# Kernel tuning notes

Hardware: AMD Instinct MI355X
Metric: run time of the kernel (lower is better)

The kernel has to match this reference:

```python
import jax, jax.numpy as jnp
import numpy as np

EPS = 1e-5

def _layernorm(x, g, b):
    # normalize over last (channel) axis
    mu = jnp.mean(x, axis=-1, keepdims=True)
    var = jnp.var(x, axis=-1, keepdims=True)
    return (x - mu) * jax.lax.rsqrt(var + EPS) * g + b

def _dynamix(xt, wnd, bnd, wnn, bnn):
    # xt: [B, M, N, C]; mixes over the N axis (vectorized form of the per-slice loop)
    B, M, N, C = xt.shape
    d = wnd.shape[1]
    p = xt @ wnd + bnd                       # [B,M,N,d]
    p = p.reshape(B, M, N * d) @ wnn + bnn   # [B,M,N*N]
    p = jax.nn.softmax(p.reshape(B, M, N, N), axis=-1)
    return jnp.einsum('bmij,bmjc->bmic', p, xt)  # [B,M,N,C]

def setup_inputs() -> dict:
    key = jax.random.key(0)
    ks = jax.random.split(key, 10)
    B, C, H, W, d, E = 32, 128, 56, 56, 10, 4
    def n(k, shape, scale=0.02):
        return jax.random.normal(k, shape, jnp.float32) * scale
    return {
        'x': jax.random.normal(ks[0], (B, C, H, W), jnp.float32),
        'ln1_g': jnp.ones((C,), jnp.float32), 'ln1_b': jnp.zeros((C,), jnp.float32),
        'h_wnd': n(ks[1], (C, d)), 'h_bnd': jnp.zeros((d,), jnp.float32),
        'h_wnn': n(ks[2], (W * d, W * W)), 'h_bnn': jnp.zeros((W * W,), jnp.float32),
        'w_wnd': n(ks[3], (C, d)), 'w_bnd': jnp.zeros((d,), jnp.float32),
        'w_wnn': n(ks[4], (H * d, H * H)), 'w_bnn': jnp.zeros((H * H,), jnp.float32),
        'pc_w': n(ks[5], (C, C)), 'pc_b': jnp.zeros((C,), jnp.float32),
        'po_w': n(ks[6], (C, C)), 'po_b': jnp.zeros((C,), jnp.float32),
        'ln2_g': jnp.ones((C,), jnp.float32), 'ln2_b': jnp.zeros((C,), jnp.float32),
        'fc1_w': n(ks[7], (C, E * C)), 'fc1_b': jnp.zeros((E * C,), jnp.float32),
        'fc2_w': n(ks[8], (E * C, C)), 'fc2_b': jnp.zeros((C,), jnp.float32),
    }

def reference(x, ln1_g, ln1_b, h_wnd, h_bnd, h_wnn, h_bnn,
              w_wnd, w_bnd, w_wnn, w_bnn, pc_w, pc_b, po_w, po_b,
              ln2_g, ln2_b, fc1_w, fc1_b, fc2_w, fc2_b):
    # x: [B,C,H,W] -> work channels-last [B,H,W,C]
    xt = jnp.transpose(x, (0, 2, 3, 1))
    # ---- block p1: LN + DynaMixer ----
    u = _layernorm(xt, ln1_g, ln1_b)                 # [B,H,W,C]
    y_h = _dynamix(u, h_wnd, h_bnd, h_wnn, h_bnn)    # mix over W per row
    u_w = jnp.transpose(u, (0, 2, 1, 3))             # [B,W,H,C]
    y_w = _dynamix(u_w, w_wnd, w_bnd, w_wnn, w_bnn)  # mix over H per col
    y_w = jnp.transpose(y_w, (0, 2, 1, 3))           # back to [B,H,W,C]
    y_c = u @ pc_w + pc_b                            # 1x1 conv proj_c
    y = (y_h + y_w + y_c) @ po_w + po_b              # 1x1 conv proj_o
    xt = xt + y                                      # residual (drop_path=0)
    # ---- block p2: LN + MLP ----
    v = _layernorm(xt, ln2_g, ln2_b)
    h = jax.nn.gelu(v @ fc1_w + fc1_b, approximate=False)
    h = h @ fc2_w + fc2_b
    xt = xt + h
    return jnp.transpose(xt, (0, 3, 1, 2))           # [B,C,H,W]
```

## Files before the change

### kernel.cpp

```cpp
#include <hip/hip_runtime.h>
#include <math.h>

#define BB 32
#define CC 128
#define HH 56
#define WW 56
#define HWHW 3136
#define TOK 100352
#define BH 1792
#define NDP 576
#define NNP 3200

typedef __attribute__((ext_vector_type(8))) short bhalf8;
typedef __attribute__((ext_vector_type(4))) float f32x4;
typedef __attribute__((ext_vector_type(4))) unsigned int u32x4;

__device__ inline unsigned short f2bf(float f) {
  unsigned int x = __float_as_uint(f);
  unsigned int r = (x + 0x7FFFu + ((x >> 16) & 1u)) >> 16;
  return (unsigned short)r;
}
__device__ inline float bf2f(unsigned short u) {
  return __uint_as_float(((unsigned int)u) << 16);
}
__device__ inline unsigned int pack2(float a, float b) {
  return (unsigned int)f2bf(a) | ((unsigned int)f2bf(b) << 16);
}
__device__ inline f32x4 MFMA(bhalf8 a, bhalf8 b, f32x4 c) {
  return __builtin_amdgcn_mfma_f32_16x16x32_bf16(a, b, c, 0, 0, 0);
}
template <int CH>
__device__ inline bhalf8 ldsFrag(const unsigned short* base, int row, int chunk) {
  return *reinterpret_cast<const bhalf8*>(base + row * (CH * 8) + ((chunk ^ (row & 7)) * 8));
}
__device__ inline float gelu_f(float x) {
  float x3 = x * x * x;
  float z = 0.7978845608028654f * (x + 0.044715f * x3);
  float e = __expf(2.0f * z);
  float t = 1.0f - 2.0f / (e + 1.0f);
  return 0.5f * x * (1.0f + t);
}

__global__ __launch_bounds__(256) void wcvt_kernel(
    const float* __restrict__ hwnn, const float* __restrict__ wwnn,
    const float* __restrict__ pcw, const float* __restrict__ pow_,
    const float* __restrict__ fc1w, const float* __restrict__ fc2w,
    const float* __restrict__ hwnd, const float* __restrict__ wwnd,
    unsigned short* __restrict__ wnnTh, unsigned short* __restrict__ wnnTw,
    unsigned short* __restrict__ pcT, unsigned short* __restrict__ poT,
    unsigned short* __restrict__ fc1T, unsigned short* __restrict__ fc2T,
    unsigned short* __restrict__ wcatT, u32x4* __restrict__ pdzero) {
  int gt = blockIdx.x * 256 + threadIdx.x;
  int gs = gridDim.x * 256;
  for (int i = gt; i < 258048; i += gs) { u32x4 z = {0, 0, 0, 0}; pdzero[i] = z; }
  for (int i = gt; i < 3200 * 576; i += gs) {
    int k = i / 3200, n = i % 3200;
    float v = (n < 3136 && k < 560) ? hwnn[(size_t)k * 3136 + n] : 0.f;
    wnnTh[(size_t)n * 576 + k] = f2bf(v);
  }
  for (int i = gt; i < 3200 * 576; i += gs) {
    int k = i / 3200, n = i % 3200;
    float v = (n < 3136 && k < 560) ? wwnn[(size_t)k * 3136 + n] : 0.f;
    wnnTw[(size_t)n * 576 + k] = f2bf(v);
  }
  for (int i = gt; i < 128 * 128; i += gs) { int k = i >> 7, n = i & 127; pcT[n * 128 + k] = f2bf(pcw[i]); }
  for (int i = gt; i < 128 * 128; i += gs) { int k = i >> 7, n = i & 127; poT[n * 128 + k] = f2bf(pow_[i]); }
  for (int i = gt; i < 128 * 512; i += gs) { int k = i >> 9, n = i & 511; fc1T[n * 128 + k] = f2bf(fc1w[i]); }
  for (int i = gt; i < 512 * 128; i += gs) { int k = i >> 7, n = i & 127; fc2T[n * 512 + k] = f2bf(fc2w[i]); }
  for (int i = gt; i < 128 * 32; i += gs) {
    int k = i >> 5, n = i & 31;
    float v = n < 10 ? hwnd[k * 10 + n] : (n < 20 ? wwnd[k * 10 + (n - 10)] : 0.f);
    wcatT[n * 128 + k] = f2bf(v);
  }
}

__global__ __launch_bounds__(256) void ln1_kernel(const float* __restrict__ x,
    const float* __restrict__ g, const float* __restrict__ bt,
    unsigned short* __restrict__ ubf, unsigned short* __restrict__ xcl) {
  int bh = blockIdx.x;
  int b = bh / HH, h = bh % HH;
  __shared__ float lds[WW][CC + 1];
  __shared__ float mu[WW], rs[WW];
  const float* xp = x + ((size_t)b * CC) * HWHW + (size_t)h * WW;
  for (int idx = threadIdx.x; idx < CC * WW; idx += 256) {
    int c = idx / WW, w = idx % WW;
    lds[w][c] = xp[(size_t)c * HWHW + w];
  }
  __syncthreads();
  if (threadIdx.x < WW) {
    int w = threadIdx.x;
    float s = 0.f, ss = 0.f;
    for (int c = 0; c < CC; ++c) { float v = lds[w][c]; s += v; ss += v * v; }
    float m = s * (1.0f / CC);
    float var = ss * (1.0f / CC) - m * m;
    mu[w] = m; rs[w] = rsqrtf(var + 1e-5f);
  }
  __syncthreads();
  unsigned short* up = ubf + (size_t)bh * (WW * CC);
  unsigned short* xc = xcl + (size_t)bh * (WW * CC);
  for (int idx = threadIdx.x; idx < WW * CC; idx += 256) {
    int w = idx >> 7, c = idx & 127;
    float v = lds[w][c];
    up[idx] = f2bf((v - mu[w]) * rs[w] * g[c] + bt[c]);
    xc[idx] = f2bf(v);
  }
}

__global__ __launch_bounds__(256) void pd_mfma(const unsigned short* __restrict__ ubf,
    const unsigned short* __restrict__ wcatT, const float* __restrict__ hbnd,
    const float* __restrict__ wbnd, unsigned short* __restrict__ pdh,
    unsigned short* __restrict__ pdw) {
  __shared__ __align__(16) unsigned short sU[64 * 128];
  __shared__ __align__(16) unsigned short sW[32 * 128];
  int tid = threadIdx.x;
  int tok0 = blockIdx.x * 64;
  #pragma unroll
  for (int i = 0; i < 4; ++i) {
    int s = i * 256 + tid; int r = s >> 4, c = s & 15;
    u32x4 v = *reinterpret_cast<const u32x4*>(ubf + (size_t)(tok0 + r) * 128 + c * 8);
    *reinterpret_cast<u32x4*>(sU + r * 128 + ((c ^ (r & 7)) * 8)) = v;
  }
  #pragma unroll
  for (int i = 0; i < 2; ++i) {
    int s = i * 256 + tid; int r = s >> 4, c = s & 15;
    u32x4 v = *reinterpret_cast<const u32x4*>(wcatT + (size_t)r * 128 + c * 8);
    *reinterpret_cast<u32x4*>(sW + r * 128 + ((c ^ (r & 7)) * 8)) = v;
  }
  __syncthreads();
  int wid = tid >> 6, lane = tid & 63, l16 = lane & 15, lk = lane >> 4;
  f32x4 acc[2] = {};
  #pragma unroll
  for (int kk = 0; kk < 4; ++kk) {
    bhalf8 a = ldsFrag<16>(sU, wid * 16 + l16, kk * 4 + lk);
    #pragma unroll
    for (int f = 0; f < 2; ++f) {
      bhalf8 b = ldsFrag<16>(sW, f * 16 + l16, kk * 4 + lk);
      acc[f] = MFMA(a, b, acc[f]);
    }
  }
  #pragma unroll
  for (int f = 0; f < 2; ++f) {
    int n = f * 16 + l16;
    #pragma unroll
    for (int r = 0; r < 4; ++r) {
      int tok = tok0 + wid * 16 + lk * 4 + r;
      float v = acc[f][r];
      if (n < 10) {
        pdh[((size_t)(tok / 56)) * NDP + (size_t)(tok % 56) * 10 + n] = f2bf(v + hbnd[n]);
      } else if (n < 20) {
        int b = tok / HWHW; int rem = tok % HWHW; int hh = rem / 56; int w = rem % 56;
        pdw[((size_t)(b * 56 + w)) * NDP + (size_t)hh * 10 + (n - 10)] = f2bf(v + wbnd[n - 10]);
      }
    }
  }
}

__global__ __launch_bounds__(256) void gemm_logits(
    const unsigned short* __restrict__ A, const unsigned short* __restrict__ BT,
    const float* __restrict__ bias, unsigned short* __restrict__ Cout) {
  __shared__ __align__(16) unsigned short sA[128 * 64];
  __shared__ __align__(16) unsigned short sB[128 * 64];
  int tid = threadIdx.x;
  int row0 = blockIdx.y * 128, col0 = blockIdx.x * 128;
  int wid = tid >> 6, lane = tid & 63;
  int wm = wid >> 1, wn = wid & 1;
  int l16 = lane & 15, lk = lane >> 4;
  f32x4 acc[4][4] = {};
  for (int k0 = 0; k0 < NDP; k0 += 64) {
    #pragma unroll
    for (int i = 0; i < 4; ++i) {
      int s = i * 256 + tid; int r = s >> 3, c = s & 7;
      u32x4 v = *reinterpret_cast<const u32x4*>(A + (size_t)(row0 + r) * NDP + k0 + c * 8);
      *reinterpret_cast<u32x4*>(sA + r * 64 + ((c ^ (r & 7)) * 8)) = v;
    }
    #pragma unroll
    for (int i = 0; i < 4; ++i) {
      int s = i * 256 + tid; int r = s >> 3, c = s & 7;
      u32x4 v = *reinterpret_cast<const u32x4*>(BT + (size_t)(col0 + r) * NDP + k0 + c * 8);
      *reinterpret_cast<u32x4*>(sB + r * 64 + ((c ^ (r & 7)) * 8)) = v;
    }
    __syncthreads();
    bhalf8 af[4][2], bf[4][2];
    #pragma unroll
    for (int f = 0; f < 4; ++f)
      #pragma unroll
      for (int kk = 0; kk < 2; ++kk) {
        af[f][kk] = ldsFrag<8>(sA, wm * 64 + f * 16 + l16, kk * 4 + lk);
        bf[f][kk] = ldsFrag<8>(sB, wn * 64 + f * 16 + l16, kk * 4 + lk);
      }
    #pragma unroll
    for (int i = 0; i < 4; ++i)
      #pragma unroll
      for (int j = 0; j < 4; ++j) {
        acc[i][j] = MFMA(af[i][0], bf[j][0], acc[i][j]);
        acc[i][j] = MFMA(af[i][1], bf[j][1], acc[i][j]);
      }
    __syncthreads();
  }
  #pragma unroll
  for (int i = 0; i < 4; ++i) {
    int rbase = row0 + wm * 64 + i * 16 + lk * 4;
    #pragma unroll
    for (int j = 0; j < 4; ++j) {
      int col = col0 + wn * 64 + j * 16 + l16;
      if (col < HWHW) {
        float bv = bias[col];
        #pragma unroll
        for (int r = 0; r < 4; ++r)
          Cout[(size_t)(rbase + r) * NNP + col] = f2bf(acc[i][j][r] + bv);
      }
    }
  }
}

__global__ __launch_bounds__(256) void softmax56_kernel(unsigned short* __restrict__ ph,
                                                        unsigned short* __restrict__ pw) {
  int wave = (blockIdx.x * 256 + threadIdx.x) >> 6;
  int lane = threadIdx.x & 63;
  if (wave >= 2 * TOK) return;
  unsigned short* buf = wave < TOK ? ph : pw;
  int row = wave < TOK ? wave : wave - TOK;
  int bh = row / 56, i = row % 56;
  unsigned short* p = buf + (size_t)bh * NNP + (size_t)i * 56;
  float xv = lane < WW ? bf2f(p[lane]) : -INFINITY;
  float m = xv;
  for (int o = 32; o > 0; o >>= 1) m = fmaxf(m, __shfl_xor(m, o));
  float e = lane < WW ? __expf(xv - m) : 0.f;
  float s = e;
  for (int o = 32; o > 0; o >>= 1) s += __shfl_xor(s, o);
  if (lane < WW) p[lane] = f2bf(e / s);
}

__global__ __launch_bounds__(256) void mixh_pc(const unsigned short* __restrict__ ph,
    const unsigned short* __restrict__ ubf, const unsigned short* __restrict__ pcT,
    const float* __restrict__ pcb, unsigned short* __restrict__ accm) {
  int bh = blockIdx.x;
  int tok0 = bh * 56;
  __shared__ __align__(16) unsigned short sP[64 * 64];
  __shared__ __align__(16) unsigned short sUn[64 * 128];
  __shared__ __align__(16) unsigned short sUt[128 * 64];
  __shared__ __align__(16) unsigned short pcL[128 * 128];
  int tid = threadIdx.x;
  for (int s = tid; s < 512; s += 256) {
    int r = s >> 3, c = s & 7;
    u32x4 v = {0, 0, 0, 0};
    if (r < 56 && c < 7) v = *reinterpret_cast<const u32x4*>(ph + (size_t)bh * NNP + r * 56 + c * 8);
    *reinterpret_cast<u32x4*>(sP + r * 64 + ((c ^ (r & 7)) * 8)) = v;
  }
  for (int s = tid; s < 1024; s += 256) {
    int r = s >> 4, c = s & 15;
    u32x4 v = {0, 0, 0, 0};
    if (r < 56) v = *reinterpret_cast<const u32x4*>(ubf + (size_t)(tok0 + r) * 128 + c * 8);
    *reinterpret_cast<u32x4*>(sUn + r * 128 + ((c ^ (r & 7)) * 8)) = v;
  }
  for (int s = tid; s < 1024; s += 256) {
    int j = s >> 4, cc = s & 15;
    unsigned short e8[8] = {0, 0, 0, 0, 0, 0, 0, 0};
    if (j < 56)
      *reinterpret_cast<u32x4*>(e8) =
          *reinterpret_cast<const u32x4*>(ubf + (size_t)(tok0 + j) * 128 + cc * 8);
    #pragma unroll
    for (int e = 0; e < 8; ++e) {
      int cf = cc * 8 + e;
      sUt[cf * 64 + (((j >> 3) ^ (cf & 7)) * 8) + (j & 7)] = e8[e];
    }
  }
  for (int s = tid; s < 2048; s += 256) {
    int r = s >> 4, c = s & 15;
    u32x4 v = *reinterpret_cast<const u32x4*>(pcT + (size_t)r * 128 + c * 8);
    *reinterpret_cast<u32x4*>(pcL + r * 128 + ((c ^ (r & 7)) * 8)) = v;
  }
  __syncthreads();
  int lane = tid & 63, l16 = lane & 15, lk = lane >> 4, wn = tid >> 6;
  f32x4 acc[4][2] = {};
  #pragma unroll
  for (int kk = 0; kk < 2; ++kk) {
    bhalf8 a[4], b[2];
    #pragma unroll
    for (int i = 0; i < 4; ++i) a[i] = ldsFrag<8>(sP, i * 16 + l16, kk * 4 + lk);
    #pragma unroll
    for (int j = 0; j < 2; ++j) b[j] = ldsFrag<8>(sUt, wn * 32 + j * 16 + l16, kk * 4 + lk);
    #pragma unroll
    for (int i = 0; i < 4; ++i)
      #pragma unroll
      for (int j = 0; j < 2; ++j) acc[i][j] = MFMA(a[i], b[j], acc[i][j]);
  }
  #pragma unroll
  for (int kk = 0; kk < 4; ++kk) {
    bhalf8 a[4], b[2];
    #pragma unroll
    for (int i = 0; i < 4; ++i) a[i] = ldsFrag<16>(sUn, i * 16 + l16, kk * 4 + lk);
    #pragma unroll
    for (int j = 0; j < 2; ++j) b[j] = ldsFrag<16>(pcL, wn * 32 + j * 16 + l16, kk * 4 + lk);
    #pragma unroll
    for (int i = 0; i < 4; ++i)
      #pragma unroll
      for (int j = 0; j < 2; ++j) acc[i][j] = MFMA(a[i], b[j], acc[i][j]);
  }
  #pragma unroll
  for (int i = 0; i < 4; ++i) {
    int tok = i * 16 + lk * 4;
    #pragma unroll
    for (int j = 0; j < 2; ++j) {
      int c = wn * 32 + j * 16 + l16;
      float bv = pcb[c];
      #pragma unroll
      for (int r = 0; r < 4; ++r)
        if (tok + r < 56)
          accm[(size_t)(tok0 + tok + r) * 128 + c] = f2bf(acc[i][j][r] + bv);
    }
  }
}

__global__ __launch_bounds__(256) void mixw_fin(const unsigned short* __restrict__ pw,
    const unsigned short* __restrict__ ubf, const unsigned short* __restrict__ poT,
    const float* __restrict__ pob, const unsigned short* __restrict__ xcl,
    unsigned short* __restrict__ accXt) {
  int bw = blockIdx.x;
  int bq = bw / 56, w = bw % 56;
  __shared__ __align__(16) unsigned short sP[64 * 64];
  __shared__ __align__(16) unsigned short sUt[128 * 64];
  __shared__ __align__(16) unsigned short sS[64 * 128];
  __shared__ __align__(16) unsigned short poL[128 * 128];
  int tid = threadIdx.x;
  for (int s = tid; s < 512; s += 256) {
    int r = s >> 3, c = s & 7;
    u32x4 v = {0, 0, 0, 0};
    if (r < 56 && c < 7) v = *reinterpret_cast<const u32x4*>(pw + (size_t)bw * NNP + r * 56 + c * 8);
    *reinterpret_cast<u32x4*>(sP + r * 64 + ((c ^ (r & 7)) * 8)) = v;
  }
  for (int s = tid; s < 1024; s += 256) {
    int j = s >> 4, cc = s & 15;
    unsigned short e8[8] = {0, 0, 0, 0, 0, 0, 0, 0};
    if (j < 56)
      *reinterpret_cast<u32x4*>(e8) =
          *reinterpret_cast<const u32x4*>(ubf + ((size_t)bq * HWHW + (size_t)j * 56 + w) * 128 + cc * 8);
    #pragma unroll
    for (int e = 0; e < 8; ++e) {
      int cf = cc * 8 + e;
      sUt[cf * 64 + (((j >> 3) ^ (cf & 7)) * 8) + (j & 7)] = e8[e];
    }
  }
  for (int s = tid; s < 1024; s += 256) {
    int r = s >> 4, c = s & 15;
    u32x4 v = {0, 0, 0, 0};
    if (r < 56) v = *reinterpret_cast<const u32x4*>(accXt + ((size_t)bq * HWHW + (size_t)r * 56 + w) * 128 + c * 8);
    *reinterpret_cast<u32x4*>(sS + r * 128 + ((c ^ (r & 7)) * 8)) = v;
  }
  for (int s = tid; s < 2048; s += 256) {
    int r = s >> 4, c = s & 15;
    u32x4 v = *reinterpret_cast<const u32x4*>(poT + (size_t)r * 128 + c * 8);
    *reinterpret_cast<u32x4*>(poL + r * 128 + ((c ^ (r & 7)) * 8)) = v;
  }
  __syncthreads();
  int lane = tid & 63, l16 = lane & 15, lk = lane >> 4, wn = tid >> 6;
  f32x4 acc1[4][2] = {};
  #pragma unroll
  for (int kk = 0; kk < 2; ++kk) {
    bhalf8 a[4], b[2];
    #pragma unroll
    for (int i = 0; i < 4; ++i) a[i] = ldsFrag<8>(sP, i * 16 + l16, kk * 4 + lk);
    #pragma unroll
    for (int j = 0; j < 2; ++j) b[j] = ldsFrag<8>(sUt, wn * 32 + j * 16 + l16, kk * 4 + lk);
    #pragma unroll
    for (int i = 0; i < 4; ++i)
      #pragma unroll
      for (int j = 0; j < 2; ++j) acc1[i][j] = MFMA(a[i], b[j], acc1[i][j]);
  }
  #pragma unroll
  for (int i = 0; i < 4; ++i) {
    #pragma unroll
    for (int j = 0; j < 2; ++j) {
      int col = wn * 32 + j * 16 + l16;
      #pragma unroll
      for (int r = 0; r < 4; ++r) {
        int row = i * 16 + lk * 4 + r;
        int ad = row * 128 + (((col >> 3) ^ (row & 7)) * 8) + (col & 7);
        sS[ad] = f2bf(bf2f(sS[ad]) + acc1[i][j][r]);
      }
    }
  }
  __syncthreads();
  f32x4 acc2[4][2] = {};
  #pragma unroll
  for (int kk = 0; kk < 4; ++kk) {
    bhalf8 a[4], b[2];
    #pragma unroll
    for (int i = 0; i < 4; ++i) a[i] = ldsFrag<16>(sS, i * 16 + l16, kk * 4 + lk);
    #pragma unroll
    for (int j = 0; j < 2; ++j) b[j] = ldsFrag<16>(poL, wn * 32 + j * 16 + l16, kk * 4 + lk);
    #pragma unroll
    for (int i = 0; i < 4; ++i)
      #pragma unroll
      for (int j = 0; j < 2; ++j) acc2[i][j] = MFMA(a[i], b[j], acc2[i][j]);
  }
  #pragma unroll
  for (int i = 0; i < 4; ++i) {
    #pragma unroll
    for (int j = 0; j < 2; ++j) {
      int c = wn * 32 + j * 16 + l16;
      float bv = pob[c];
      #pragma unroll
      for (int r = 0; r < 4; ++r) {
        int row = i * 16 + lk * 4 + r;
        if (row < 56) {
          size_t t = (size_t)bq * HWHW + (size_t)row * 56 + w;
          float z = acc2[i][j][r] + bv + bf2f(xcl[t * 128 + c]);
          accXt[t * 128 + c] = f2bf(z);
        }
      }
    }
  }
}

__global__ __launch_bounds__(256) void mlp2(const unsigned short* __restrict__ xt2,
    const unsigned short* __restrict__ w1T, const float* __restrict__ b1,
    const unsigned short* __restrict__ w2T, const float* __restrict__ b2,
    const float* __restrict__ g, const float* __restrict__ bt,
    float* __restrict__ out) {
  __shared__ __align__(16) char smem[65536];
  unsigned short* sV = (unsigned short*)smem;
  unsigned short* sW = (unsigned short*)(smem + 16384);
  unsigned short* sH = (unsigned short*)(smem + 49152);
  float* T = (float*)(smem + 16384);
  __shared__ float b1s[512];
  __shared__ float gls[128], bls[128], b2s[128];
  __shared__ float psum[64][4], psq[64][4];
  __shared__ float mus[64], rss[64];
  int tid = threadIdx.x;
  int tok0 = blockIdx.x * 64;
  if (tid < 128) { gls[tid] = g[tid]; bls[tid] = bt[tid]; b2s[tid] = b2[tid]; }
  for (int i = tid; i < 512; i += 256) b1s[i] = b1[i];
  for (int s = tid; s < 1024; s += 256) {
    int r = s >> 4, c = s & 15;
    u32x4 v = *reinterpret_cast<const u32x4*>(xt2 + (size_t)(tok0 + r) * 128 + c * 8);
    #pragma unroll
    for (int e = 0; e < 4; ++e) {
      T[r * 129 + c * 8 + 2 * e]     = bf2f((unsigned short)(v[e] & 0xFFFFu));
      T[r * 129 + c * 8 + 2 * e + 1] = bf2f((unsigned short)(v[e] >> 16));
    }
  }
  __syncthreads();
  {
    int t = tid & 63, q = tid >> 6;
    float s1 = 0.f, s2 = 0.f;
    #pragma unroll 8
    for (int i = 0; i < 32; ++i) { float v = T[t * 129 + q * 32 + i]; s1 += v; s2 += v * v; }
    psum[t][q] = s1; psq[t][q] = s2;
  }
  __syncthreads();
  if (tid < 64) {
    float s1 = psum[tid][0] + psum[tid][1] + psum[tid][2] + psum[tid][3];
    float s2 = psq[tid][0] + psq[tid][1] + psq[tid][2] + psq[tid][3];
    float m = s1 * (1.0f / CC);
    float var = s2 * (1.0f / CC) - m * m;
    mus[tid] = m; rss[tid] = rsqrtf(var + 1e-5f);
  }
  __syncthreads();
  for (int s = tid; s < 1024; s += 256) {
    int r = s >> 4, c = s & 15;
    float m = mus[r], rv = rss[r];
    unsigned int wds[4];
    #pragma unroll
    for (int e = 0; e < 4; ++e) {
      int c0 = c * 8 + 2 * e;
      float v0 = (T[r * 129 + c0]     - m) * rv * gls[c0]     + bls[c0];
      float v1 = (T[r * 129 + c0 + 1] - m) * rv * gls[c0 + 1] + bls[c0 + 1];
      wds[e] = pack2(v0, v1);
    }
    u32x4 v = {wds[0], wds[1], wds[2], wds[3]};
    *reinterpret_cast<u32x4*>(sV + r * 128 + ((c ^ (r & 7)) * 8)) = v;
  }
  __syncthreads();
  int lane = tid & 63, l16 = lane & 15, lk = lane >> 4, wid = tid >> 6;
  int wmA = wid >> 1, wnA = wid & 1;
  int wc = wid >> 1, wt = wid & 1;
  f32x4 acc2[4][2] = {};
  for (int hc = 0; hc < 4; ++hc) {
    for (int s = tid; s < 2048; s += 256) {
      int r = s >> 4, c = s & 15;
      u32x4 v = *reinterpret_cast<const u32x4*>(w1T + (size_t)(hc * 128 + r) * 128 + c * 8);
      *reinterpret_cast<u32x4*>(sW + r * 128 + ((c ^ (r & 7)) * 8)) = v;
    }
    __syncthreads();
    f32x4 acc1[2][4] = {};
    #pragma unroll
    for (int kk = 0; kk < 4; ++kk) {
      bhalf8 a[2], b[4];
      #pragma unroll
      for (int i = 0; i < 2; ++i) a[i] = ldsFrag<16>(sV, wmA * 32 + i * 16 + l16, kk * 4 + lk);
      #pragma unroll
      for (int j = 0; j < 4; ++j) b[j] = ldsFrag<16>(sW, wnA * 64 + j * 16 + l16, kk * 4 + lk);
      #pragma unroll
      for (int i = 0; i < 2; ++i)
        #pragma unroll
        for (int j = 0; j < 4; ++j) acc1[i][j] = MFMA(a[i], b[j], acc1[i][j]);
    }
    #pragma unroll
    for (int i = 0; i < 2; ++i) {
      #pragma unroll
      for (int j = 0; j < 4; ++j) {
        int hid = wnA * 64 + j * 16 + l16;
        float bv = b1s[hc * 128 + hid];
        #pragma unroll
        for (int r = 0; r < 4; ++r) {
          int tok = wmA * 32 + i * 16 + lk * 4 + r;
          float hval = gelu_f(acc1[i][j][r] + bv);
          sH[tok * 128 + (((hid >> 3) ^ (tok & 7)) * 8) + (hid & 7)] = f2bf(hval);
        }
      }
    }
    __syncthreads();
    for (int s = tid; s < 2048; s += 256) {
      int r = s >> 4, c = s & 15;
      u32x4 v = *reinterpret_cast<const u32x4*>(w2T + (size_t)r * 512 + hc * 128 + c * 8);
      *reinterpret_cast<u32x4*>(sW + r * 128 + ((c ^ (r & 7)) * 8)) = v;
    }
    __syncthreads();
    #pragma unroll
    for (int kk = 0; kk < 4; ++kk) {
      bhalf8 a[4], b[2];
      #pragma unroll
      for (int i = 0; i < 4; ++i) a[i] = ldsFrag<16>(sW, wc * 64 + i * 16 + l16, kk * 4 + lk);
      #pragma unroll
      for (int j = 0; j < 2; ++j) b[j] = ldsFrag<16>(sH, wt * 32 + j * 16 + l16, kk * 4 + lk);
      #pragma unroll
      for (int i = 0; i < 4; ++i)
        #pragma unroll
        for (int j = 0; j < 2; ++j) acc2[i][j] = MFMA(a[i], b[j], acc2[i][j]);
    }
    __syncthreads();
  }
  #pragma unroll
  for (int i = 0; i < 4; ++i) {
    #pragma unroll
    for (int j = 0; j < 2; ++j) {
      int tok = wt * 32 + j * 16 + l16;
      #pragma unroll
      for (int r = 0; r < 4; ++r) {
        int c = wc * 64 + i * 16 + lk * 4 + r;
        T[tok * 129 + c] = acc2[i][j][r];
      }
    }
  }
  __syncthreads();
  for (int s = tid; s < 1024; s += 256) {
    int r = s >> 4, c = s & 15;
    u32x4 v = *reinterpret_cast<const u32x4*>(xt2 + (size_t)(tok0 + r) * 128 + c * 8);
    #pragma unroll
    for (int e = 0; e < 4; ++e) {
      int c0 = c * 8 + 2 * e;
      T[r * 129 + c0]     += bf2f((unsigned short)(v[e] & 0xFFFFu)) + b2s[c0];
      T[r * 129 + c0 + 1] += bf2f((unsigned short)(v[e] >> 16))     + b2s[c0 + 1];
    }
  }
  __syncthreads();
  int bq = tok0 / HWHW;
  int pos0 = tok0 % HWHW;
  for (int s = tid; s < 8192; s += 256) {
    int c = s >> 6, t = s & 63;
    out[((size_t)(bq * CC + c)) * HWHW + pos0 + t] = T[t * 129 + c];
  }
}

extern "C" void kernel_launch(void* const* d_in, const int* in_sizes, int n_in,
                              void* d_out, int out_size, void* d_ws, size_t ws_size,
                              hipStream_t stream) {
  const float* x     = (const float*)d_in[0];
  const float* ln1_g = (const float*)d_in[1];
  const float* ln1_b = (const float*)d_in[2];
  const float* h_wnd = (const float*)d_in[3];
  const float* h_bnd = (const float*)d_in[4];
  const float* h_wnn = (const float*)d_in[5];
  const float* h_bnn = (const float*)d_in[6];
  const float* w_wnd = (const float*)d_in[7];
  const float* w_bnd = (const float*)d_in[8];
  const float* w_wnn = (const float*)d_in[9];
  const float* w_bnn = (const float*)d_in[10];
  const float* pc_w  = (const float*)d_in[11];
  const float* pc_b  = (const float*)d_in[12];
  const float* po_w  = (const float*)d_in[13];
  const float* po_b  = (const float*)d_in[14];
  const float* ln2_g = (const float*)d_in[15];
  const float* ln2_b = (const float*)d_in[16];
  const float* fc1_w = (const float*)d_in[17];
  const float* fc1_b = (const float*)d_in[18];
  const float* fc2_w = (const float*)d_in[19];
  const float* fc2_b = (const float*)d_in[20];
  float* out = (float*)d_out;
  char* ws = (char*)d_ws;

  unsigned short* ubf   = (unsigned short*)(ws + 0);
  unsigned short* xcl   = (unsigned short*)(ws + 25690112);
  unsigned short* accXt = (unsigned short*)(ws + 51380224);
  unsigned short* pdh   = (unsigned short*)(ws + 77070336);
  unsigned short* pdw   = (unsigned short*)(ws + 79134720);
  unsigned short* ph    = (unsigned short*)(ws + 81199104);
  unsigned short* pw    = (unsigned short*)(ws + 92667904);
  unsigned short* wnnTh = (unsigned short*)(ws + 104136704);
  unsigned short* wnnTw = (unsigned short*)(ws + 107823104);
  unsigned short* pcT   = (unsigned short*)(ws + 111509504);
  unsigned short* poT   = (unsigned short*)(ws + 111542272);
  unsigned short* fc1T  = (unsigned short*)(ws + 111575040);
  unsigned short* fc2T  = (unsigned short*)(ws + 111706112);
  unsigned short* wcatT = (unsigned short*)(ws + 111837184);

  wcvt_kernel<<<2048, 256, 0, stream>>>(h_wnn, w_wnn, pc_w, po_w, fc1_w, fc2_w,
      h_wnd, w_wnd, wnnTh, wnnTw, pcT, poT, fc1T, fc2T, wcatT, (u32x4*)pdh);
  ln1_kernel<<<BH, 256, 0, stream>>>(x, ln1_g, ln1_b, ubf, xcl);
  pd_mfma<<<TOK / 64, 256, 0, stream>>>(ubf, wcatT, h_bnd, w_bnd, pdh, pdw);
  gemm_logits<<<dim3(NNP / 128, BH / 128), 256, 0, stream>>>(pdh, wnnTh, h_bnn, ph);
  gemm_logits<<<dim3(NNP / 128, BH / 128), 256, 0, stream>>>(pdw, wnnTw, w_bnn, pw);
  softmax56_kernel<<<(2 * TOK) / 4, 256, 0, stream>>>(ph, pw);
  mixh_pc<<<BH, 256, 0, stream>>>(ph, ubf, pcT, pc_b, accXt);
  mixw_fin<<<BB * WW, 256, 0, stream>>>(pw, ubf, poT, po_b, xcl, accXt);
  mlp2<<<TOK / 64, 256, 0, stream>>>(accXt, fc1T, fc1_b, fc2T, fc2_b, ln2_g, ln2_b, out);
}
```

Measured before the change: 332.4 us.

## Fuse LN1 with projection, fold softmax into mix kernels, split LN2 out of MLP

Merges the LayerNorm-1 kernel with the small d-projection MFMA so the normalized row tile is reused from LDS instead of being reread from global memory. The standalone softmax pass over the logits is removed and done in shared memory inside the mixing kernels, which saves a full read-modify-write of both logit buffers. LayerNorm-2 moves out of the MLP kernel into a separate wave-per-token kernel that writes a bf16 buffer reusing ubf. This adds one kernel launch and an extra write and read of the normalized activations, in exchange for less LDS work and fewer barriers in the MLP kernel.

After: 369.6 us. +11.2%, slower.

```diff
diff --git a/kernel.cpp b/kernel.cpp
--- a/kernel.cpp
+++ b/kernel.cpp
@@ -74,21 +74,37 @@
   }
 }
 
-__global__ __launch_bounds__(256) void ln1_kernel(const float* __restrict__ x,
+__global__ __launch_bounds__(256) void ln1pd_kernel(const float* __restrict__ x,
     const float* __restrict__ g, const float* __restrict__ bt,
-    unsigned short* __restrict__ ubf, unsigned short* __restrict__ xcl) {
+    const unsigned short* __restrict__ wcatT, const float* __restrict__ hbnd,
+    const float* __restrict__ wbnd,
+    unsigned short* __restrict__ ubf, unsigned short* __restrict__ xcl,
+    unsigned short* __restrict__ pdh, unsigned short* __restrict__ pdw) {
   int bh = blockIdx.x;
   int b = bh / HH, h = bh % HH;
   __shared__ float lds[WW][CC + 1];
   __shared__ float mu[WW], rs[WW];
+  __shared__ __align__(16) unsigned short sUb[64 * 128];
+  __shared__ __align__(16) unsigned short sWc[32 * 128];
+  int tid = threadIdx.x;
   const float* xp = x + ((size_t)b * CC) * HWHW + (size_t)h * WW;
-  for (int idx = threadIdx.x; idx < CC * WW; idx += 256) {
+  for (int idx = tid; idx < CC * WW; idx += 256) {
     int c = idx / WW, w = idx % WW;
     lds[w][c] = xp[(size_t)c * HWHW + w];
   }
-  __syncthreads();
-  if (threadIdx.x < WW) {
-    int w = threadIdx.x;
+  #pragma unroll
+  for (int i = 0; i < 2; ++i) {
+    int s = i * 256 + tid; int r = s >> 4, c = s & 15;
+    u32x4 v = *reinterpret_cast<const u32x4*>(wcatT + (size_t)r * 128 + c * 8);
+    *reinterpret_cast<u32x4*>(sWc + r * 128 + ((c ^ (r & 7)) * 8)) = v;
+  }
+  if (tid < 128) {
+    u32x4 z = {0, 0, 0, 0};
+    *reinterpret_cast<u32x4*>(sUb + 56 * 128 + tid * 8) = z;
+  }
+  __syncthreads();
+  if (tid < WW) {
+    int w = tid;
     float s = 0.f, ss = 0.f;
     for (int c = 0; c < CC; ++c) { float v = lds[w][c]; s += v; ss += v * v; }
     float m = s * (1.0f / CC);
@@ -98,44 +114,33 @@
   __syncthreads();
   unsigned short* up = ubf + (size_t)bh * (WW * CC);
   unsigned short* xc = xcl + (size_t)bh * (WW * CC);
-  for (int idx = threadIdx.x; idx < WW * CC; idx += 256) {
-    int w = idx >> 7, c = idx & 127;
-    float v = lds[w][c];
-    up[idx] = f2bf((v - mu[w]) * rs[w] * g[c] + bt[c]);
-    xc[idx] = f2bf(v);
-  }
-}
-
-__global__ __launch_bounds__(256) void pd_mfma(const unsigned short* __restrict__ ubf,
-    const unsigned short* __restrict__ wcatT, const float* __restrict__ hbnd,
-    const float* __restrict__ wbnd, unsigned short* __restrict__ pdh,
-    unsigned short* __restrict__ pdw) {
-  __shared__ __align__(16) unsigned short sU[64 * 128];
-  __shared__ __align__(16) unsigned short sW[32 * 128];
-  int tid = threadIdx.x;
-  int tok0 = blockIdx.x * 64;
-  #pragma unroll
-  for (int i = 0; i < 4; ++i) {
-    int s = i * 256 + tid; int r = s >> 4, c = s & 15;
-    u32x4 v = *reinterpret_cast<const u32x4*>(ubf + (size_t)(tok0 + r) * 128 + c * 8);
-    *reinterpret_cast<u32x4*>(sU + r * 128 + ((c ^ (r & 7)) * 8)) = v;
-  }
-  #pragma unroll
-  for (int i = 0; i < 2; ++i) {
-    int s = i * 256 + tid; int r = s >> 4, c = s & 15;
-    u32x4 v = *reinterpret_cast<const u32x4*>(wcatT + (size_t)r * 128 + c * 8);
-    *reinterpret_cast<u32x4*>(sW + r * 128 + ((c ^ (r & 7)) * 8)) = v;
+  for (int s = tid; s < 896; s += 256) {
+    int w = s >> 4, cg = s & 15;
+    float m = mu[w], rv = rs[w];
+    unsigned int uw[4], xw[4];
+    #pragma unroll
+    for (int e = 0; e < 4; ++e) {
+      int c0 = cg * 8 + 2 * e;
+      float v0 = lds[w][c0], v1 = lds[w][c0 + 1];
+      uw[e] = pack2((v0 - m) * rv * g[c0] + bt[c0], (v1 - m) * rv * g[c0 + 1] + bt[c0 + 1]);
+      xw[e] = pack2(v0, v1);
+    }
+    u32x4 uv = {uw[0], uw[1], uw[2], uw[3]};
+    u32x4 xv = {xw[0], xw[1], xw[2], xw[3]};
+    *reinterpret_cast<u32x4*>(up + w * 128 + cg * 8) = uv;
+    *reinterpret_cast<u32x4*>(xc + w * 128 + cg * 8) = xv;
+    *reinterpret_cast<u32x4*>(sUb + w * 128 + ((cg ^ (w & 7)) * 8)) = uv;
   }
   __syncthreads();
   int wid = tid >> 6, lane = tid & 63, l16 = lane & 15, lk = lane >> 4;
   f32x4 acc[2] = {};
   #pragma unroll
   for (int kk = 0; kk < 4; ++kk) {
-    bhalf8 a = ldsFrag<16>(sU, wid * 16 + l16, kk * 4 + lk);
+    bhalf8 a = ldsFrag<16>(sUb, wid * 16 + l16, kk * 4 + lk);
     #pragma unroll
     for (int f = 0; f < 2; ++f) {
-      bhalf8 b = ldsFrag<16>(sW, f * 16 + l16, kk * 4 + lk);
-      acc[f] = MFMA(a, b, acc[f]);
+      bhalf8 bv = ldsFrag<16>(sWc, f * 16 + l16, kk * 4 + lk);
+      acc[f] = MFMA(a, bv, acc[f]);
     }
   }
   #pragma unroll
@@ -143,13 +148,14 @@
     int n = f * 16 + l16;
     #pragma unroll
     for (int r = 0; r < 4; ++r) {
-      int tok = tok0 + wid * 16 + lk * 4 + r;
-      float v = acc[f][r];
-      if (n < 10) {
-        pdh[((size_t)(tok / 56)) * NDP + (size_t)(tok % 56) * 10 + n] = f2bf(v + hbnd[n]);
-      } else if (n < 20) {
-        int b = tok / HWHW; int rem = tok % HWHW; int hh = rem / 56; int w = rem % 56;
-        pdw[((size_t)(b * 56 + w)) * NDP + (size_t)hh * 10 + (n - 10)] = f2bf(v + wbnd[n - 10]);
+      int w = wid * 16 + lk * 4 + r;
+      if (w < 56) {
+        float v = acc[f][r];
+        if (n < 10) {
+          pdh[(size_t)bh * NDP + (size_t)w * 10 + n] = f2bf(v + hbnd[n]);
+        } else if (n < 20) {
+          pdw[((size_t)(b * 56 + w)) * NDP + (size_t)h * 10 + (n - 10)] = f2bf(v + wbnd[n - 10]);
+        }
       }
     }
   }
@@ -213,22 +219,19 @@
   }
 }
 
-__global__ __launch_bounds__(256) void softmax56_kernel(unsigned short* __restrict__ ph,
-                                                        unsigned short* __restrict__ pw) {
-  int wave = (blockIdx.x * 256 + threadIdx.x) >> 6;
-  int lane = threadIdx.x & 63;
-  if (wave >= 2 * TOK) return;
-  unsigned short* buf = wave < TOK ? ph : pw;
-  int row = wave < TOK ? wave : wave - TOK;
-  int bh = row / 56, i = row % 56;
-  unsigned short* p = buf + (size_t)bh * NNP + (size_t)i * 56;
-  float xv = lane < WW ? bf2f(p[lane]) : -INFINITY;
-  float m = xv;
-  for (int o = 32; o > 0; o >>= 1) m = fmaxf(m, __shfl_xor(m, o));
-  float e = lane < WW ? __expf(xv - m) : 0.f;
-  float s = e;
-  for (int o = 32; o > 0; o >>= 1) s += __shfl_xor(s, o);
-  if (lane < WW) p[lane] = f2bf(e / s);
+__device__ inline void softmax_tile(unsigned short* sP, int tid) {
+  int wid = tid >> 6, lane = tid & 63;
+  for (int r = wid; r < 56; r += 4) {
+    float v = lane < 56 ? bf2f(sP[r * 64 + lane]) : -1e30f;
+    float m = v;
+    for (int o = 32; o > 0; o >>= 1) m = fmaxf(m, __shfl_xor(m, o));
+    float e = lane < 56 ? __expf(v - m) : 0.f;
+    float ssum = e;
+    for (int o = 32; o > 0; o >>= 1) ssum += __shfl_xor(ssum, o);
+    float p = e / ssum;
+    int pos = r * 64 + ((((lane >> 3) ^ (r & 7))) << 3) + (lane & 7);
+    sP[pos] = lane < 56 ? f2bf(p) : (unsigned short)0;
+  }
 }
 
 __global__ __launch_bounds__(256) void mixh_pc(const unsigned short* __restrict__ ph,
@@ -245,7 +248,7 @@
     int r = s >> 3, c = s & 7;
     u32x4 v = {0, 0, 0, 0};
     if (r < 56 && c < 7) v = *reinterpret_cast<const u32x4*>(ph + (size_t)bh * NNP + r * 56 + c * 8);
-    *reinterpret_cast<u32x4*>(sP + r * 64 + ((c ^ (r & 7)) * 8)) = v;
+    *reinterpret_cast<u32x4*>(sP + r * 64 + c * 8) = v;
   }
   for (int s = tid; s < 1024; s += 256) {
     int r = s >> 4, c = s & 15;
@@ -270,6 +273,8 @@
     u32x4 v = *reinterpret_cast<const u32x4*>(pcT + (size_t)r * 128 + c * 8);
     *reinterpret_cast<u32x4*>(pcL + r * 128 + ((c ^ (r & 7)) * 8)) = v;
   }
+  __syncthreads();
+  softmax_tile(sP, tid);
   __syncthreads();
   int lane = tid & 63, l16 = lane & 15, lk = lane >> 4, wn = tid >> 6;
   f32x4 acc[4][2] = {};
@@ -327,7 +332,7 @@
     int r = s >> 3, c = s & 7;
     u32x4 v = {0, 0, 0, 0};
     if (r < 56 && c < 7) v = *reinterpret_cast<const u32x4*>(pw + (size_t)bw * NNP + r * 56 + c * 8);
-    *reinterpret_cast<u32x4*>(sP + r * 64 + ((c ^ (r & 7)) * 8)) = v;
+    *reinterpret_cast<u32x4*>(sP + r * 64 + c * 8) = v;
   }
   for (int s = tid; s < 1024; s += 256) {
     int j = s >> 4, cc = s & 15;
@@ -352,6 +357,8 @@
     u32x4 v = *reinterpret_cast<const u32x4*>(poT + (size_t)r * 128 + c * 8);
     *reinterpret_cast<u32x4*>(poL + r * 128 + ((c ^ (r & 7)) * 8)) = v;
   }
+  __syncthreads();
+  softmax_tile(sP, tid);
   __syncthreads();
   int lane = tid & 63, l16 = lane & 15, lk = lane >> 4, wn = tid >> 6;
   f32x4 acc1[4][2] = {};
@@ -413,10 +420,31 @@
   }
 }
 
-__global__ __launch_bounds__(256) void mlp2(const unsigned short* __restrict__ xt2,
+__global__ __launch_bounds__(256) void ln2_kernel(const unsigned short* __restrict__ xt2,
+    const float* __restrict__ g, const float* __restrict__ bt,
+    unsigned short* __restrict__ vbf) {
+  int wave = (blockIdx.x * 256 + threadIdx.x) >> 6;
+  int lane = threadIdx.x & 63;
+  if (wave >= TOK) return;
+  const unsigned short* xp = xt2 + (size_t)wave * CC;
+  unsigned int wrd = *reinterpret_cast<const unsigned int*>(xp + lane * 2);
+  float a = bf2f((unsigned short)(wrd & 0xFFFFu));
+  float b2v = bf2f((unsigned short)(wrd >> 16));
+  float s = a + b2v, ss = a * a + b2v * b2v;
+  for (int o = 32; o > 0; o >>= 1) { s += __shfl_xor(s, o); ss += __shfl_xor(ss, o); }
+  float m = s * (1.0f / CC);
+  float var = ss * (1.0f / CC) - m * m;
+  float rv = rsqrtf(var + 1e-5f);
+  int c0 = lane * 2;
+  float n0 = (a - m) * rv * g[c0] + bt[c0];
+  float n1 = (b2v - m) * rv * g[c0 + 1] + bt[c0 + 1];
+  *reinterpret_cast<unsigned int*>(vbf + (size_t)wave * CC + c0) = pack2(n0, n1);
+}
+
+__global__ __launch_bounds__(256) void mlp2(const unsigned short* __restrict__ vbf,
+    const unsigned short* __restrict__ xt2,
     const unsigned short* __restrict__ w1T, const float* __restrict__ b1,
     const unsigned short* __restrict__ w2T, const float* __restrict__ b2,
-    const float* __restrict__ g, const float* __restrict__ bt,
     float* __restrict__ out) {
   __shared__ __align__(16) char smem[65536];
   unsigned short* sV = (unsigned short*)smem;
@@ -424,51 +452,14 @@
   unsigned short* sH = (unsigned short*)(smem + 49152);
   float* T = (float*)(smem + 16384);
   __shared__ float b1s[512];
-  __shared__ float gls[128], bls[128], b2s[128];
-  __shared__ float psum[64][4], psq[64][4];
-  __shared__ float mus[64], rss[64];
+  __shared__ float b2s[128];
   int tid = threadIdx.x;
   int tok0 = blockIdx.x * 64;
-  if (tid < 128) { gls[tid] = g[tid]; bls[tid] = bt[tid]; b2s[tid] = b2[tid]; }
+  if (tid < 128) b2s[tid] = b2[tid];
   for (int i = tid; i < 512; i += 256) b1s[i] = b1[i];
   for (int s = tid; s < 1024; s += 256) {
     int r = s >> 4, c = s & 15;
-    u32x4 v = *reinterpret_cast<const u32x4*>(xt2 + (size_t)(tok0 + r) * 128 + c * 8);
-    #pragma unroll
-    for (int e = 0; e < 4; ++e) {
-      T[r * 129 + c * 8 + 2 * e]     = bf2f((unsigned short)(v[e] & 0xFFFFu));
-      T[r * 129 + c * 8 + 2 * e + 1] = bf2f((unsigned short)(v[e] >> 16));
-    }
-  }
-  __syncthreads();
-  {
-    int t = tid & 63, q = tid >> 6;
-    float s1 = 0.f, s2 = 0.f;
-    #pragma unroll 8
-    for (int i = 0; i < 32; ++i) { float v = T[t * 129 + q * 32 + i]; s1 += v; s2 += v * v; }
-    psum[t][q] = s1; psq[t][q] = s2;
-  }
-  __syncthreads();
-  if (tid < 64) {
-    float s1 = psum[tid][0] + psum[tid][1] + psum[tid][2] + psum[tid][3];
-    float s2 = psq[tid][0] + psq[tid][1] + psq[tid][2] + psq[tid][3];
-    float m = s1 * (1.0f / CC);
-    float var = s2 * (1.0f / CC) - m * m;
-    mus[tid] = m; rss[tid] = rsqrtf(var + 1e-5f);
-  }
-  __syncthreads();
-  for (int s = tid; s < 1024; s += 256) {
-    int r = s >> 4, c = s & 15;
-    float m = mus[r], rv = rss[r];
-    unsigned int wds[4];
-    #pragma unroll
-    for (int e = 0; e < 4; ++e) {
-      int c0 = c * 8 + 2 * e;
-      float v0 = (T[r * 129 + c0]     - m) * rv * gls[c0]     + bls[c0];
-      float v1 = (T[r * 129 + c0 + 1] - m) * rv * gls[c0 + 1] + bls[c0 + 1];
-      wds[e] = pack2(v0, v1);
-    }
-    u32x4 v = {wds[0], wds[1], wds[2], wds[3]};
+    u32x4 v = *reinterpret_cast<const u32x4*>(vbf + (size_t)(tok0 + r) * 128 + c * 8);
     *reinterpret_cast<u32x4*>(sV + r * 128 + ((c ^ (r & 7)) * 8)) = v;
   }
   __syncthreads();
@@ -604,15 +595,16 @@
   unsigned short* fc1T  = (unsigned short*)(ws + 111575040);
   unsigned short* fc2T  = (unsigned short*)(ws + 111706112);
   unsigned short* wcatT = (unsigned short*)(ws + 111837184);
+  unsigned short* vbf   = ubf;
 
   wcvt_kernel<<<2048, 256, 0, stream>>>(h_wnn, w_wnn, pc_w, po_w, fc1_w, fc2_w,
       h_wnd, w_wnd, wnnTh, wnnTw, pcT, poT, fc1T, fc2T, wcatT, (u32x4*)pdh);
-  ln1_kernel<<<BH, 256, 0, stream>>>(x, ln1_g, ln1_b, ubf, xcl);
-  pd_mfma<<<TOK / 64, 256, 0, stream>>>(ubf, wcatT, h_bnd, w_bnd, pdh, pdw);
+  ln1pd_kernel<<<BH, 256, 0, stream>>>(x, ln1_g, ln1_b, wcatT, h_bnd, w_bnd,
+      ubf, xcl, pdh, pdw);
   gemm_logits<<<dim3(NNP / 128, BH / 128), 256, 0, stream>>>(pdh, wnnTh, h_bnn, ph);
   gemm_logits<<<dim3(NNP / 128, BH / 128), 256, 0, stream>>>(pdw, wnnTw, w_bnn, pw);
-  softmax56_kernel<<<(2 * TOK) / 4, 256, 0, stream>>>(ph, pw);
   mixh_pc<<<BH, 256, 0, stream>>>(ph, ubf, pcT, pc_b, accXt);
   mixw_fin<<<BB * WW, 256, 0, stream>>>(pw, ubf, poT, po_b, xcl, accXt);
-  mlp2<<<TOK / 64, 256, 0, stream>>>(accXt, fc1T, fc1_b, fc2T, fc2_b, ln2_g, ln2_b, out);
-}
+  ln2_kernel<<<TOK / 4, 256, 0, stream>>>(accXt, ln2_g, ln2_b, vbf);
+  mlp2<<<TOK / 64, 256, 0, stream>>>(vbf, accXt, fc1T, fc1_b, fc2T, fc2_b, out);
+}
```
